# Kernel tuning notes

Measured on AMD Instinct MI355X. Metric: run time of the kernel, lower is better.

## Reference

```python
import jax, jax.numpy as jnp
import numpy as np

N = 16384      # batch size
F = 1024       # n_features
H = 256        # n_dim (latent)


def setup_inputs() -> dict:
    key = jax.random.key(0)
    ks = jax.random.split(key, 6)
    X = jax.random.normal(ks[0], (N, F), dtype=jnp.float32)
    We = jax.random.normal(ks[1], (F, H), dtype=jnp.float32) / np.sqrt(F).astype(np.float32)
    be = jnp.zeros((H,), dtype=jnp.float32)
    Wd = jax.random.normal(ks[2], (H, F), dtype=jnp.float32) / np.sqrt(H).astype(np.float32)
    bd = jnp.zeros((F,), dtype=jnp.float32)
    Wc = jax.random.normal(ks[3], (H, 1), dtype=jnp.float32) / np.sqrt(H).astype(np.float32)
    bc = jnp.zeros((1,), dtype=jnp.float32)
    s = jax.random.randint(ks[4], (N,), 0, 2, dtype=jnp.int32)  # protected attribute labels in {0,1}
    return {"X": X, "We": We, "be": be, "Wd": Wd, "bd": bd, "Wc": Wc, "bc": bc, "s": s, "p": 1}


def reference(X, We, be, Wd, bd, Wc, bc, s, p):
    # encoder / decoder (single Linear each, as in the default NRL construction)
    g = X @ We + be                      # [N, H]
    rec = g @ Wd + bd                    # [N, F]
    mse_mean = jnp.mean((rec - X) ** 2)  # MSELoss is built with reduction='sum' but forward uses torch.mean(pow(...)) directly

    # critic scores for ALL rows (critics share weights: [module]*n_protected)
    c = (g @ Wc + bc)[:, 0]              # [N]

    # masked pairwise L1: sum_{i in P, j notin P} |c_i - c_j|
    mp = (s == p)                        # rows where s == p
    mpf = mp.astype(c.dtype)
    mrf = (~mp).astype(c.dtype)
    Dmat = jnp.abs(c[:, None] - c[None, :])   # [N, N] pairwise L1 (cdist equivalent)
    total = mpf @ (Dmat @ mrf)                # mp^T D mr == cdist(c_p, c_rest, p=1).sum()

    w_dist_count = mp.sum()                   # == w_dist.shape[0] (number of protected rows)
    w_dist_mean = total / w_dist_count.astype(c.dtype)

    return (mse_mean, jnp.asarray(rec.shape[0]), w_dist_mean, w_dist_count)
```

## Files before the change

kernel.cpp:

```cpp
#include <hip/hip_runtime.h>
#include <hip/hip_bf16.h>
#include <cstdint>

#define NR 16384
#define NF 1024
#define NH 256

typedef __bf16 bf16x8 __attribute__((ext_vector_type(8)));
typedef float f32x4 __attribute__((ext_vector_type(4)));
typedef unsigned short us8 __attribute__((ext_vector_type(8)));

static __device__ __forceinline__ unsigned short f2bf(float f) {
    unsigned u = __float_as_uint(f);
    u += 0x7FFFu + ((u >> 16) & 1u);
    return (unsigned short)(u >> 16);
}
static __device__ __forceinline__ unsigned cvt2(float a, float b) {
    return ((unsigned)f2bf(b) << 16) | (unsigned)f2bf(a);
}

__device__ __forceinline__ void gl2lds16(const void* gp, void* lp) {
    __builtin_amdgcn_global_load_lds(
        (const __attribute__((address_space(1))) unsigned int*)gp,
        (__attribute__((address_space(3))) unsigned int*)lp, 16, 0, 0);
}

__global__ __launch_bounds__(256) void transpose_bf_kernel(
    const float* __restrict__ src, unsigned short* __restrict__ dst, int R, int C) {
    __shared__ float tile[32][33];
    const int c0 = blockIdx.x * 32, r0 = blockIdx.y * 32;
    const int t = threadIdx.x;
#pragma unroll
    for (int p = 0; p < 4; p++) {
        int idx = t + 256 * p;
        int r = idx >> 5, c = idx & 31;
        tile[r][c] = src[(size_t)(r0 + r) * C + c0 + c];
    }
    __syncthreads();
#pragma unroll
    for (int p = 0; p < 4; p++) {
        int idx = t + 256 * p;
        int rr = idx & 31, cc = idx >> 5;
        dst[(size_t)(c0 + cc) * R + r0 + rr] = f2bf(tile[rr][cc]);
    }
}

__global__ __launch_bounds__(256) void gemm1_kernel(
    const float* __restrict__ X, const unsigned short* __restrict__ WeT,
    const float* __restrict__ be, const float* __restrict__ Wc,
    unsigned short* __restrict__ g, float* __restrict__ cpart) {
    __shared__ float As[2][32 * 32];
    __shared__ unsigned short Bs[2][256 * 32];
    __shared__ float credu[4][32];
    const int t = threadIdx.x;
    const int m0 = blockIdx.x * 32;
    const int w = t >> 6, lane = t & 63, q = lane >> 4, li = lane & 15;
    const int nw = w * 64;

    const int ar = t >> 3, acx = (t & 7) ^ (ar & 7);
    const float* Ag = X + (size_t)(m0 + ar) * NF + acx * 4;
    const int br = t >> 2, bcx = (t & 3) ^ ((br >> 1) & 3);
    const unsigned short* Bg = WeT + (size_t)br * NF + bcx * 8;

    f32x4 acc[2][4] = {};

    gl2lds16(Ag, &As[0][t * 4]);
#pragma unroll
    for (int p = 0; p < 4; p++)
        gl2lds16(Bg + (size_t)(64 * p) * NF, &Bs[0][(t + 256 * p) * 8]);

    for (int it = 0; it < 32; ++it) {
        const int cur = it & 1;
        __syncthreads();
        if (it + 1 < 32) {
            const int k1 = (it + 1) * 32;
            gl2lds16(Ag + k1, &As[cur ^ 1][t * 4]);
#pragma unroll
            for (int p = 0; p < 4; p++)
                gl2lds16(Bg + (size_t)(64 * p) * NF + k1, &Bs[cur ^ 1][(t + 256 * p) * 8]);
        }
        bf16x8 af[2], bfv[4];
#pragma unroll
        for (int i = 0; i < 2; i++) {
            int r = i * 16 + li;
            int s0 = (2 * q) ^ (r & 7);
            f32x4 lo = *(const f32x4*)&As[cur][r * 32 + s0 * 4];
            f32x4 hi = *(const f32x4*)&As[cur][r * 32 + (s0 ^ 1) * 4];
            uint4 pk;
            pk.x = cvt2(lo[0], lo[1]); pk.y = cvt2(lo[2], lo[3]);
            pk.z = cvt2(hi[0], hi[1]); pk.w = cvt2(hi[2], hi[3]);
            af[i] = __builtin_bit_cast(bf16x8, pk);
        }
#pragma unroll
        for (int j = 0; j < 4; j++) {
            int r = nw + j * 16 + li;
            int s = q ^ ((r >> 1) & 3);
            bfv[j] = __builtin_bit_cast(bf16x8, *(const us8*)&Bs[cur][r * 32 + s * 8]);
        }
#pragma unroll
        for (int i = 0; i < 2; i++)
#pragma unroll
            for (int j = 0; j < 4; j++)
                acc[i][j] = __builtin_amdgcn_mfma_f32_16x16x32_bf16(bfv[j], af[i], acc[i][j], 0, 0, 0);
    }

#pragma unroll
    for (int i = 0; i < 2; i++) {
        float csum = 0.f;
#pragma unroll
        for (int j = 0; j < 4; j++) {
            int colb = nw + j * 16 + q * 4;
            float4 be4 = *(const float4*)&be[colb];
            float4 wc4 = *(const float4*)&Wc[colb];
            float v0 = acc[i][j][0] + be4.x;
            float v1 = acc[i][j][1] + be4.y;
            float v2 = acc[i][j][2] + be4.z;
            float v3 = acc[i][j][3] + be4.w;
            csum += v0 * wc4.x + v1 * wc4.y + v2 * wc4.z + v3 * wc4.w;
            ushort4 st = { f2bf(v0), f2bf(v1), f2bf(v2), f2bf(v3) };
            *(ushort4*)&g[(size_t)(m0 + i * 16 + li) * NH + colb] = st;
        }
        csum += __shfl_down(csum, 32);
        csum += __shfl_down(csum, 16);
        if (lane < 16) credu[w][i * 16 + lane] = csum;
    }
    __syncthreads();
    if (t < 32)
        cpart[m0 + t] = credu[0][t] + credu[1][t] + credu[2][t] + credu[3][t];
}

__global__ __launch_bounds__(256) void gemm2_kernel(
    const unsigned short* __restrict__ g, const unsigned short* __restrict__ WdT,
    const float* __restrict__ bd, const float* __restrict__ X,
    float* __restrict__ mseparts) {
    __shared__ unsigned short As[2][64 * 32];
    __shared__ unsigned short Bs[2][128 * 32];
    __shared__ float msred[4];
    const int t = threadIdx.x;
    const int m0 = blockIdx.x * 64;
    const int n0 = blockIdx.y * 128;
    const int w = t >> 6, lane = t & 63, q = lane >> 4, li = lane & 15;
    const int wr = (w >> 1) * 32, wn = (w & 1) * 64;

    const int r2 = t >> 2, c2 = (t & 3) ^ ((r2 >> 1) & 3);
    const unsigned short* Ag = g + (size_t)(m0 + r2) * NH + c2 * 8;
    const unsigned short* Bg = WdT + (size_t)(n0 + r2) * NH + c2 * 8;

    f32x4 acc[2][4] = {};

    gl2lds16(Ag, &As[0][t * 8]);
    gl2lds16(Bg, &Bs[0][t * 8]);
    gl2lds16(Bg + (size_t)64 * NH, &Bs[0][(t + 256) * 8]);

    for (int it = 0; it < 8; ++it) {
        const int cur = it & 1;
        __syncthreads();
        if (it + 1 < 8) {
            const int k1 = (it + 1) * 32;
            gl2lds16(Ag + k1, &As[cur ^ 1][t * 8]);
            gl2lds16(Bg + k1, &Bs[cur ^ 1][t * 8]);
            gl2lds16(Bg + (size_t)64 * NH + k1, &Bs[cur ^ 1][(t + 256) * 8]);
        }
        bf16x8 af[2], bfv[4];
#pragma unroll
        for (int i = 0; i < 2; i++) {
            int r = wr + i * 16 + li;
            int s = q ^ ((r >> 1) & 3);
            af[i] = __builtin_bit_cast(bf16x8, *(const us8*)&As[cur][r * 32 + s * 8]);
        }
#pragma unroll
        for (int j = 0; j < 4; j++) {
            int r = wn + j * 16 + li;
            int s = q ^ ((r >> 1) & 3);
            bfv[j] = __builtin_bit_cast(bf16x8, *(const us8*)&Bs[cur][r * 32 + s * 8]);
        }
#pragma unroll
        for (int i = 0; i < 2; i++)
#pragma unroll
            for (int j = 0; j < 4; j++)
                acc[i][j] = __builtin_amdgcn_mfma_f32_16x16x32_bf16(bfv[j], af[i], acc[i][j], 0, 0, 0);
    }

    float lsum = 0.f;
#pragma unroll
    for (int i = 0; i < 2; i++) {
        const size_t rowoff = (size_t)(m0 + wr + i * 16 + li) * NF;
#pragma unroll
        for (int j = 0; j < 4; j++) {
            int colb = n0 + wn + j * 16 + q * 4;
            float4 bd4 = *(const float4*)&bd[colb];
            float4 xr = *(const float4*)&X[rowoff + colb];
            float d0 = acc[i][j][0] + bd4.x - xr.x;
            float d1 = acc[i][j][1] + bd4.y - xr.y;
            float d2 = acc[i][j][2] + bd4.z - xr.z;
            float d3 = acc[i][j][3] + bd4.w - xr.w;
            lsum += d0 * d0 + d1 * d1 + d2 * d2 + d3 * d3;
        }
    }
#pragma unroll
    for (int o = 32; o; o >>= 1) lsum += __shfl_down(lsum, o);
    if (lane == 0) msred[w] = lsum;
    __syncthreads();
    if (t == 0)
        atomicAdd(&mseparts[(blockIdx.x * 8 + blockIdx.y) & 63],
                  msred[0] + msred[1] + msred[2] + msred[3]);
}

__global__ __launch_bounds__(256) void compact_kernel(
    const float* __restrict__ c, const int* __restrict__ s, const int* __restrict__ pv,
    float* __restrict__ cP, float* __restrict__ cR, int* __restrict__ cnt) {
    int i = blockIdx.x * 256 + threadIdx.x;
    float ci = c[i];
    bool pr = (s[i] == pv[0]);
    int lane = threadIdx.x & 63;
    unsigned long long m = __ballot(pr);
    {
        int cm = __popcll(m);
        int base = 0;
        if (lane == 0 && cm) base = atomicAdd(&cnt[0], cm);
        base = __shfl(base, 0);
        int off = __popcll(m & ((1ull << lane) - 1ull));
        if (pr) cP[base + off] = ci;
    }
    {
        unsigned long long mm = ~m;
        int cm = __popcll(mm);
        int base = 0;
        if (lane == 0 && cm) base = atomicAdd(&cnt[1], cm);
        base = __shfl(base, 0);
        int off = __popcll(mm & ((1ull << lane) - 1ull));
        if (!pr) cR[base + off] = ci;
    }
}

__global__ __launch_bounds__(256) void pair_kernel(
    const float* __restrict__ cP, const float* __restrict__ cR,
    const int* __restrict__ cnt, float* __restrict__ pairparts) {
    __shared__ float sj[1024];
    const int nP = cnt[0], nR = cnt[1];
    const int jb = blockIdx.x * 1024;
    int jn = nR - jb; if (jn < 0) jn = 0; if (jn > 1024) jn = 1024;
    for (int j = threadIdx.x; j < 1024; j += 256)
        sj[j] = (jb + j < nR) ? cR[jb + j] : 0.f;
    __syncthreads();
    const int a0 = blockIdx.y * 512 + threadIdx.x;
    const int a1 = a0 + 256;
    const float ca0 = (a0 < nP) ? cP[a0] : 0.f;
    const float ca1 = (a1 < nP) ? cP[a1] : 0.f;
    float s0 = 0.f, s1 = 0.f;
#pragma unroll 4
    for (int j4 = 0; j4 < 256; j4++) {
        float4 v = *(const float4*)&sj[j4 * 4];
        s0 += fabsf(ca0 - v.x) + fabsf(ca0 - v.y) + fabsf(ca0 - v.z) + fabsf(ca0 - v.w);
        s1 += fabsf(ca1 - v.x) + fabsf(ca1 - v.y) + fabsf(ca1 - v.z) + fabsf(ca1 - v.w);
    }
    float pad = (float)(1024 - jn);
    s0 -= pad * fabsf(ca0);
    s1 -= pad * fabsf(ca1);
    if (a0 >= nP) s0 = 0.f;
    if (a1 >= nP) s1 = 0.f;
    float s = s0 + s1;
#pragma unroll
    for (int o = 32; o; o >>= 1) s += __shfl_down(s, o);
    if ((threadIdx.x & 63) == 0)
        atomicAdd(&pairparts[((blockIdx.y << 4) ^ blockIdx.x ^ (threadIdx.x >> 6)) & 63], s);
}

__global__ void finalize_kernel(const float* __restrict__ mseparts,
                                const float* __restrict__ pairparts,
                                const int* __restrict__ cnt, float* __restrict__ out) {
    float ms = 0.f, ps = 0.f;
    for (int i = 0; i < 64; i++) { ms += mseparts[i]; ps += pairparts[i]; }
    out[0] = ms / (float)((size_t)NR * NF);
    out[1] = (float)NR;
    out[2] = ps / (float)cnt[0];
    out[3] = (float)cnt[0];
}

extern "C" void kernel_launch(void* const* d_in, const int* in_sizes, int n_in,
                              void* d_out, int out_size, void* d_ws, size_t ws_size,
                              hipStream_t stream) {
    const float* X  = (const float*)d_in[0];
    const float* We = (const float*)d_in[1];
    const float* be = (const float*)d_in[2];
    const float* Wd = (const float*)d_in[3];
    const float* bd = (const float*)d_in[4];
    const float* Wc = (const float*)d_in[5];
    const int*   s  = (const int*)d_in[7];
    const int*   pv = (const int*)d_in[8];

    char* ws = (char*)d_ws;
    float* mseparts  = (float*)(ws + 0);
    float* pairparts = (float*)(ws + 256);
    int*   cnt       = (int*)(ws + 512);
    float* cpart     = (float*)(ws + 1024);
    float* cP        = (float*)(ws + 1024 + 65536);
    float* cR        = (float*)(ws + 1024 + 2 * 65536);
    unsigned short* gbf = (unsigned short*)(ws + 1024 + 3 * 65536);
    unsigned short* WeT = gbf + (size_t)NR * NH;
    unsigned short* WdT = WeT + (size_t)NH * NF;

    (void)hipMemsetAsync(d_ws, 0, 1024, stream);
    transpose_bf_kernel<<<dim3(8, 32), 256, 0, stream>>>(We, WeT, 1024, 256);
    transpose_bf_kernel<<<dim3(32, 8), 256, 0, stream>>>(Wd, WdT, 256, 1024);
    gemm1_kernel<<<512, 256, 0, stream>>>(X, WeT, be, Wc, gbf, cpart);
    gemm2_kernel<<<dim3(256, 8), 256, 0, stream>>>(gbf, WdT, bd, X, mseparts);
    compact_kernel<<<64, 256, 0, stream>>>(cpart, s, pv, cP, cR, cnt);
    pair_kernel<<<dim3(16, 32), 256, 0, stream>>>(cP, cR, cnt, pairparts);
    finalize_kernel<<<1, 1, 0, stream>>>(mseparts, pairparts, cnt, (float*)d_out);
}
```

Before: 205.0 us.

## Fuse encoder and decoder GEMMs keeping latent tile in shared memory

Merges gemm1 and gemm2 into one kernel: each block computes a 32-row latent tile, stores it swizzled in LDS (aliased over the first-stage buffers via a union), then loops over all 1024 output columns streaming WdT tiles to compute the reconstruction MSE. This removes the global write and re-read of the bf16 latent matrix and one kernel launch. The cost is only 512 blocks with small 32-row tiles in the second GEMM, so WdT is re-streamed by every block and MFMA utilization per block may be lower than the separate 64x128 tiling.

```diff
diff --git a/kernel.cpp b/kernel.cpp
--- a/kernel.cpp
+++ b/kernel.cpp
@@ -45,13 +45,18 @@
     }
 }
 
-__global__ __launch_bounds__(256) void gemm1_kernel(
+__global__ __launch_bounds__(256) void fused_kernel(
     const float* __restrict__ X, const unsigned short* __restrict__ WeT,
-    const float* __restrict__ be, const float* __restrict__ Wc,
-    unsigned short* __restrict__ g, float* __restrict__ cpart) {
-    __shared__ float As[2][32 * 32];
-    __shared__ unsigned short Bs[2][256 * 32];
+    const unsigned short* __restrict__ WdT,
+    const float* __restrict__ be, const float* __restrict__ bd,
+    const float* __restrict__ Wc,
+    float* __restrict__ cpart, float* __restrict__ mseparts) {
+    __shared__ union {
+        struct { float As[2][32 * 32]; unsigned short Bs[2][256 * 32]; } p1;
+        struct { unsigned short gs[32 * 256]; unsigned short Bs2[2][128 * 32]; } p2;
+    } sh;
     __shared__ float credu[4][32];
+    __shared__ float msred[4];
     const int t = threadIdx.x;
     const int m0 = blockIdx.x * 32;
     const int w = t >> 6, lane = t & 63, q = lane >> 4, li = lane & 15;
@@ -63,29 +68,28 @@
     const unsigned short* Bg = WeT + (size_t)br * NF + bcx * 8;
 
     f32x4 acc[2][4] = {};
-
-    gl2lds16(Ag, &As[0][t * 4]);
+    gl2lds16(Ag, &sh.p1.As[0][t * 4]);
 #pragma unroll
     for (int p = 0; p < 4; p++)
-        gl2lds16(Bg + (size_t)(64 * p) * NF, &Bs[0][(t + 256 * p) * 8]);
+        gl2lds16(Bg + (size_t)(64 * p) * NF, &sh.p1.Bs[0][(t + 256 * p) * 8]);
 
     for (int it = 0; it < 32; ++it) {
         const int cur = it & 1;
         __syncthreads();
         if (it + 1 < 32) {
             const int k1 = (it + 1) * 32;
-            gl2lds16(Ag + k1, &As[cur ^ 1][t * 4]);
+            gl2lds16(Ag + k1, &sh.p1.As[cur ^ 1][t * 4]);
 #pragma unroll
             for (int p = 0; p < 4; p++)
-                gl2lds16(Bg + (size_t)(64 * p) * NF + k1, &Bs[cur ^ 1][(t + 256 * p) * 8]);
+                gl2lds16(Bg + (size_t)(64 * p) * NF + k1, &sh.p1.Bs[cur ^ 1][(t + 256 * p) * 8]);
         }
         bf16x8 af[2], bfv[4];
 #pragma unroll
         for (int i = 0; i < 2; i++) {
             int r = i * 16 + li;
             int s0 = (2 * q) ^ (r & 7);
-            f32x4 lo = *(const f32x4*)&As[cur][r * 32 + s0 * 4];
-            f32x4 hi = *(const f32x4*)&As[cur][r * 32 + (s0 ^ 1) * 4];
+            f32x4 lo = *(const f32x4*)&sh.p1.As[cur][r * 32 + s0 * 4];
+            f32x4 hi = *(const f32x4*)&sh.p1.As[cur][r * 32 + (s0 ^ 1) * 4];
             uint4 pk;
             pk.x = cvt2(lo[0], lo[1]); pk.y = cvt2(lo[2], lo[3]);
             pk.z = cvt2(hi[0], hi[1]); pk.w = cvt2(hi[2], hi[3]);
@@ -95,7 +99,7 @@
         for (int j = 0; j < 4; j++) {
             int r = nw + j * 16 + li;
             int s = q ^ ((r >> 1) & 3);
-            bfv[j] = __builtin_bit_cast(bf16x8, *(const us8*)&Bs[cur][r * 32 + s * 8]);
+            bfv[j] = __builtin_bit_cast(bf16x8, *(const us8*)&sh.p1.Bs[cur][r * 32 + s * 8]);
         }
 #pragma unroll
         for (int i = 0; i < 2; i++)
@@ -103,10 +107,19 @@
             for (int j = 0; j < 4; j++)
                 acc[i][j] = __builtin_amdgcn_mfma_f32_16x16x32_bf16(bfv[j], af[i], acc[i][j], 0, 0, 0);
     }
+    __syncthreads();
+
+    const int rB = t >> 2;
+    const int sB = (t & 3) ^ (rB & 3) ^ ((rB >> 2) & 3);
+    const unsigned short* Wg  = WdT + (size_t)rB * NH + sB * 8;
+    const unsigned short* Wg2 = WdT + (size_t)(rB + 64) * NH + sB * 8;
+    gl2lds16(Wg,  &sh.p2.Bs2[0][t * 8]);
+    gl2lds16(Wg2, &sh.p2.Bs2[0][(t + 256) * 8]);
 
 #pragma unroll
     for (int i = 0; i < 2; i++) {
         float csum = 0.f;
+        const int m = i * 16 + li;
 #pragma unroll
         for (int j = 0; j < 4; j++) {
             int colb = nw + j * 16 + q * 4;
@@ -118,7 +131,8 @@
             float v3 = acc[i][j][3] + be4.w;
             csum += v0 * wc4.x + v1 * wc4.y + v2 * wc4.z + v3 * wc4.w;
             ushort4 st = { f2bf(v0), f2bf(v1), f2bf(v2), f2bf(v3) };
-            *(ushort4*)&g[(size_t)(m0 + i * 16 + li) * NH + colb] = st;
+            int sl = ((colb >> 3) ^ m);
+            *(ushort4*)&sh.p2.gs[m * 256 + sl * 8 + (q & 1) * 4] = st;
         }
         csum += __shfl_down(csum, 32);
         csum += __shfl_down(csum, 16);
@@ -127,74 +141,53 @@
     __syncthreads();
     if (t < 32)
         cpart[m0 + t] = credu[0][t] + credu[1][t] + credu[2][t] + credu[3][t];
-}
-
-__global__ __launch_bounds__(256) void gemm2_kernel(
-    const unsigned short* __restrict__ g, const unsigned short* __restrict__ WdT,
-    const float* __restrict__ bd, const float* __restrict__ X,
-    float* __restrict__ mseparts) {
-    __shared__ unsigned short As[2][64 * 32];
-    __shared__ unsigned short Bs[2][128 * 32];
-    __shared__ float msred[4];
-    const int t = threadIdx.x;
-    const int m0 = blockIdx.x * 64;
-    const int n0 = blockIdx.y * 128;
-    const int w = t >> 6, lane = t & 63, q = lane >> 4, li = lane & 15;
-    const int wr = (w >> 1) * 32, wn = (w & 1) * 64;
-
-    const int r2 = t >> 2, c2 = (t & 3) ^ ((r2 >> 1) & 3);
-    const unsigned short* Ag = g + (size_t)(m0 + r2) * NH + c2 * 8;
-    const unsigned short* Bg = WdT + (size_t)(n0 + r2) * NH + c2 * 8;
-
-    f32x4 acc[2][4] = {};
-
-    gl2lds16(Ag, &As[0][t * 8]);
-    gl2lds16(Bg, &Bs[0][t * 8]);
-    gl2lds16(Bg + (size_t)64 * NH, &Bs[0][(t + 256) * 8]);
-
-    for (int it = 0; it < 8; ++it) {
-        const int cur = it & 1;
-        __syncthreads();
-        if (it + 1 < 8) {
-            const int k1 = (it + 1) * 32;
-            gl2lds16(Ag + k1, &As[cur ^ 1][t * 8]);
-            gl2lds16(Bg + k1, &Bs[cur ^ 1][t * 8]);
-            gl2lds16(Bg + (size_t)64 * NH + k1, &Bs[cur ^ 1][(t + 256) * 8]);
-        }
-        bf16x8 af[2], bfv[4];
+
+    float lsum = 0.f;
+    f32x4 acc2[2][2] = {};
+    for (int it = 0; it < 64; ++it) {
+        const int nc = it >> 3, kc = it & 7, cur = it & 1;
+        if (it) __syncthreads();
+        if (it + 1 < 64) {
+            const int nc1 = (it + 1) >> 3, kc1 = (it + 1) & 7;
+            const size_t off = (size_t)(nc1 * 128) * NH + kc1 * 32;
+            gl2lds16(Wg + off,  &sh.p2.Bs2[cur ^ 1][t * 8]);
+            gl2lds16(Wg2 + off, &sh.p2.Bs2[cur ^ 1][(t + 256) * 8]);
+        }
+        bf16x8 af[2], bfv[2];
 #pragma unroll
         for (int i = 0; i < 2; i++) {
-            int r = wr + i * 16 + li;
-            int s = q ^ ((r >> 1) & 3);
-            af[i] = __builtin_bit_cast(bf16x8, *(const us8*)&As[cur][r * 32 + s * 8]);
-        }
-#pragma unroll
-        for (int j = 0; j < 4; j++) {
-            int r = wn + j * 16 + li;
-            int s = q ^ ((r >> 1) & 3);
-            bfv[j] = __builtin_bit_cast(bf16x8, *(const us8*)&Bs[cur][r * 32 + s * 8]);
+            int m = i * 16 + li;
+            int sl = (kc * 4 + q) ^ m;
+            af[i] = __builtin_bit_cast(bf16x8, *(const us8*)&sh.p2.gs[m * 256 + sl * 8]);
+        }
+#pragma unroll
+        for (int j = 0; j < 2; j++) {
+            int r = w * 32 + j * 16 + li;
+            int s = q ^ (r & 3) ^ ((r >> 2) & 3);
+            bfv[j] = __builtin_bit_cast(bf16x8, *(const us8*)&sh.p2.Bs2[cur][r * 32 + s * 8]);
         }
 #pragma unroll
         for (int i = 0; i < 2; i++)
 #pragma unroll
-            for (int j = 0; j < 4; j++)
-                acc[i][j] = __builtin_amdgcn_mfma_f32_16x16x32_bf16(bfv[j], af[i], acc[i][j], 0, 0, 0);
-    }
-
-    float lsum = 0.f;
-#pragma unroll
-    for (int i = 0; i < 2; i++) {
-        const size_t rowoff = (size_t)(m0 + wr + i * 16 + li) * NF;
-#pragma unroll
-        for (int j = 0; j < 4; j++) {
-            int colb = n0 + wn + j * 16 + q * 4;
-            float4 bd4 = *(const float4*)&bd[colb];
-            float4 xr = *(const float4*)&X[rowoff + colb];
-            float d0 = acc[i][j][0] + bd4.x - xr.x;
-            float d1 = acc[i][j][1] + bd4.y - xr.y;
-            float d2 = acc[i][j][2] + bd4.z - xr.z;
-            float d3 = acc[i][j][3] + bd4.w - xr.w;
-            lsum += d0 * d0 + d1 * d1 + d2 * d2 + d3 * d3;
+            for (int j = 0; j < 2; j++)
+                acc2[i][j] = __builtin_amdgcn_mfma_f32_16x16x32_bf16(bfv[j], af[i], acc2[i][j], 0, 0, 0);
+        if (kc == 7) {
+#pragma unroll
+            for (int i = 0; i < 2; i++) {
+                const size_t rowoff = (size_t)(m0 + i * 16 + li) * NF;
+#pragma unroll
+                for (int j = 0; j < 2; j++) {
+                    int colb = nc * 128 + w * 32 + j * 16 + q * 4;
+                    float4 bd4 = *(const float4*)&bd[colb];
+                    float4 xr  = *(const float4*)&X[rowoff + colb];
+                    float d0 = acc2[i][j][0] + bd4.x - xr.x;
+                    float d1 = acc2[i][j][1] + bd4.y - xr.y;
+                    float d2 = acc2[i][j][2] + bd4.z - xr.z;
+                    float d3 = acc2[i][j][3] + bd4.w - xr.w;
+                    lsum += d0 * d0 + d1 * d1 + d2 * d2 + d3 * d3;
+                    acc2[i][j] = (f32x4){0.f, 0.f, 0.f, 0.f};
+                }
+            }
         }
     }
 #pragma unroll
@@ -202,8 +195,7 @@
     if (lane == 0) msred[w] = lsum;
     __syncthreads();
     if (t == 0)
-        atomicAdd(&mseparts[(blockIdx.x * 8 + blockIdx.y) & 63],
-                  msred[0] + msred[1] + msred[2] + msred[3]);
+        atomicAdd(&mseparts[blockIdx.x & 63], msred[0] + msred[1] + msred[2] + msred[3]);
 }
 
 __global__ __launch_bounds__(256) void compact_kernel(
@@ -296,15 +288,13 @@
     float* cpart     = (float*)(ws + 1024);
     float* cP        = (float*)(ws + 1024 + 65536);
     float* cR        = (float*)(ws + 1024 + 2 * 65536);
-    unsigned short* gbf = (unsigned short*)(ws + 1024 + 3 * 65536);
-    unsigned short* WeT = gbf + (size_t)NR * NH;
+    unsigned short* WeT = (unsigned short*)(ws + 1024 + 3 * 65536);
     unsigned short* WdT = WeT + (size_t)NH * NF;
 
     (void)hipMemsetAsync(d_ws, 0, 1024, stream);
     transpose_bf_kernel<<<dim3(8, 32), 256, 0, stream>>>(We, WeT, 1024, 256);
     transpose_bf_kernel<<<dim3(32, 8), 256, 0, stream>>>(Wd, WdT, 256, 1024);
-    gemm1_kernel<<<512, 256, 0, stream>>>(X, WeT, be, Wc, gbf, cpart);
-    gemm2_kernel<<<dim3(256, 8), 256, 0, stream>>>(gbf, WdT, bd, X, mseparts);
+    fused_kernel<<<512, 256, 0, stream>>>(X, WeT, WdT, be, bd, Wc, cpart, mseparts);
     compact_kernel<<<64, 256, 0, stream>>>(cpart, s, pv, cP, cR, cnt);
     pair_kernel<<<dim3(16, 32), 256, 0, stream>>>(cP, cR, cnt, pairparts);
     finalize_kernel<<<1, 1, 0, stream>>>(mseparts, pairparts, cnt, (float*)d_out);
```

After: 225.3 us. +9.9%, slower.
